# Optimization experiments

Hardware: AMD Instinct MI355X
Metric: run time of the kernel (lower is better)

## Reference

```python
import jax, jax.numpy as jnp
import numpy as np
import math

B, S, DIN = 8, 2048, 64
D, G, OUT_SEQ = 64, 5, 512
LN_EPS = 1e-5


def setup_inputs() -> dict:
    key = jax.random.key(0)
    ks = jax.random.split(key, 4)
    seq = jax.random.normal(ks[0], (B, S, DIN), dtype=jnp.float32)
    M = jax.random.uniform(ks[1], (D, DIN), minval=-0.5, maxval=0.5, dtype=jnp.float32)
    P = jax.random.uniform(ks[2], (D, D, G), minval=-0.1, maxval=0.1, dtype=jnp.float32)
    Linker = jax.random.uniform(ks[3], (S, OUT_SEQ), minval=-0.1, maxval=0.1, dtype=jnp.float32)
    ln_gamma = jnp.ones((D,), dtype=jnp.float32)
    ln_beta = jnp.zeros((D,), dtype=jnp.float32)
    return {"seq": seq, "M": M, "P": P, "Linker": Linker, "ln_gamma": ln_gamma, "ln_beta": ln_beta}


def _layer_norm(x, gamma, beta):
    mu = jnp.mean(x, axis=-1, keepdims=True)
    var = jnp.mean(jnp.square(x - mu), axis=-1, keepdims=True)
    return (x - mu) * jax.lax.rsqrt(var + LN_EPS) * gamma + beta


def reference(seq, M, P, Linker, ln_gamma, ln_beta):
    # periods[i,j,g] = i*(D*G) + j*G + g + 2 (constant buffer)
    periods = (jnp.arange(D * D * G, dtype=jnp.float32) + 2.0).reshape(D, D, G)
    k = jnp.arange(S, dtype=jnp.float32)
    # phi: (S, D, D, G) cosine basis
    phi = jnp.cos(2.0 * math.pi * k[:, None, None, None] / periods)
    # Precontract basis: W[k,i,j] = sum_g P[i,j,g] * phi[k,i,j,g]  -> (S, D, D)
    W = jnp.einsum('kijg,ijg->kij', phi, P)

    Z0 = jnp.einsum('bsd,od->bso', seq, M)          # x @ M^T, (B,S,D)
    Z = _layer_norm(Z0, ln_gamma, ln_beta)          # (B,S,D)
    # T[b,k,i] = sum_j Z[b,k,j] * W[k,i,j]
    T = jnp.einsum('bkj,kij->bki', Z, W)            # (B,S,D)
    U = jnp.einsum('bki,ko->boi', T, Linker)        # (B,OUT_SEQ,D)
    # shared residual: (x @ M^T)^T @ Linker, using pre-LayerNorm projection
    residual = jnp.einsum('bki,ko->boi', Z0, Linker)
    return U + residual
```

## Files before the change

kernel.cpp:

```cpp
#include <hip/hip_runtime.h>
#include <math.h>

#define SS 2048
#define OSQ 512
#define GG 5

typedef unsigned short u16;
typedef unsigned int u32;
typedef __attribute__((ext_vector_type(8))) short s16x8;
typedef __attribute__((ext_vector_type(4))) float v4f;
typedef __attribute__((ext_vector_type(16))) float v16f;

__device__ __forceinline__ float rcp_f(float x) {
    float r; asm("v_rcp_f32 %0, %1" : "=v"(r) : "v"(x)); return r;
}
__device__ __forceinline__ float cos_rev(float x) {
    float fr, c;
    asm("v_fract_f32 %0, %1" : "=v"(fr) : "v"(x));
    asm("v_cos_f32 %0, %1" : "=v"(c) : "v"(fr));
    return c;
}
__device__ __forceinline__ float cos01(float x) {
    float c; asm("v_cos_f32 %0, %1" : "=v"(c) : "v"(x)); return c;
}
__device__ __forceinline__ u16 f2bf(float f) {
    u32 u = __float_as_uint(f);
    return (u16)((u + 0x7FFFu + ((u >> 16) & 1u)) >> 16);
}
__device__ __forceinline__ float bf2f(u16 h) {
    return __uint_as_float((u32)h << 16);
}
__device__ __forceinline__ void gload16(const void* g, void* l) {
    __builtin_amdgcn_global_load_lds((const __attribute__((address_space(1))) void*)g,
                                     (__attribute__((address_space(3))) void*)l, 16, 0, 0);
}


__global__ __launch_bounds__(512, 1) void kF(const float* __restrict__ seq,
                                             const float* __restrict__ Mm,
                                             const float* __restrict__ P,
                                             const float* __restrict__ gamma,
                                             const float* __restrict__ beta,
                                             const float* __restrict__ Lnk,
                                             u16* __restrict__ Lt,
                                             u16* __restrict__ Vt) {
    __shared__ __align__(16) u16 SEQb[64 * 64];
    __shared__ __align__(16) u16 Mb[64 * 64];
    __shared__ __align__(16) u16 SZb[64 * 64];
    __shared__ float Z0l[64 * 68];
    __shared__ u32 Ta32[8 * 2 * 64 * 5];

    const int t = threadIdx.x;
    const int l = t & 63;
    const int w = t >> 6;
    const int k0 = blockIdx.x * 8;
    const float kf0 = (float)k0;

    const int h = w >> 2;
    const int i0 = (w & 3) * 16;
    const int i_w = i0 + (l & 15);
    const int jc_w = h * 4 + (l >> 4);

    float pr[40];
    {
        const float4* P4 = (const float4*)(P + ((size_t)i_w * 64 + jc_w * 8) * 5);
        #pragma unroll
        for (int q = 0; q < 10; ++q) {
            float4 v = P4[q];
            pr[q * 4 + 0] = v.x; pr[q * 4 + 1] = v.y; pr[q * 4 + 2] = v.z; pr[q * 4 + 3] = v.w;
        }
    }

    float lnv[8];
    #pragma unroll
    for (int j = 0; j < 8; ++j)
        lnv[j] = Lnk[(size_t)(k0 + j) * OSQ + t];

    {
        int row = t >> 3, ch = t & 7;
        int b = row >> 3, kq = row & 7;
        const float* sp = &seq[((size_t)b * SS + k0 + kq) * 64 + ch * 8];
        float4 a = *(const float4*)sp, bb4 = *(const float4*)(sp + 4);
        uint4 pk;
        pk.x = (u32)f2bf(a.x) | ((u32)f2bf(a.y) << 16);
        pk.y = (u32)f2bf(a.z) | ((u32)f2bf(a.w) << 16);
        pk.z = (u32)f2bf(bb4.x) | ((u32)f2bf(bb4.y) << 16);
        pk.w = (u32)f2bf(bb4.z) | ((u32)f2bf(bb4.w) << 16);
        *(uint4*)&SEQb[row * 64 + ((ch ^ (row & 7)) * 8)] = pk;

        const float* mp = &Mm[(size_t)row * 64 + ch * 8];
        float4 c = *(const float4*)mp, d = *(const float4*)(mp + 4);
        uint4 pm;
        pm.x = (u32)f2bf(c.x) | ((u32)f2bf(c.y) << 16);
        pm.y = (u32)f2bf(c.z) | ((u32)f2bf(c.w) << 16);
        pm.z = (u32)f2bf(d.x) | ((u32)f2bf(d.y) << 16);
        pm.w = (u32)f2bf(d.z) | ((u32)f2bf(d.w) << 16);
        *(uint4*)&Mb[row * 64 + ((ch ^ (row & 7)) * 8)] = pm;
    }

    float c0[40], c1[40], t2c[40];
    #pragma unroll
    for (int m = 0; m < 8; ++m) {
        #pragma unroll
        for (int g = 0; g < GG; ++g) {
            int idx = m * 5 + g;
            float pf = (float)((i_w * 64 + jc_w * 8 + m) * 5 + g + 2);
            float inv = rcp_f(pf);
            c0[idx] = cos_rev(kf0 * inv);
            c1[idx] = cos_rev((kf0 + 1.0f) * inv);
            float ct = cos01(inv);
            t2c[idx] = ct + ct;
        }
    }

    float gm[8], bt[8];
    {
        int oc = t & 7;
        float4 a = *(const float4*)&gamma[oc * 8], b = *(const float4*)&gamma[oc * 8 + 4];
        float4 c = *(const float4*)&beta[oc * 8],  d = *(const float4*)&beta[oc * 8 + 4];
        gm[0]=a.x; gm[1]=a.y; gm[2]=a.z; gm[3]=a.w; gm[4]=b.x; gm[5]=b.y; gm[6]=b.z; gm[7]=b.w;
        bt[0]=c.x; bt[1]=c.y; bt[2]=c.z; bt[3]=c.w; bt[4]=d.x; bt[5]=d.y; bt[6]=d.z; bt[7]=d.w;
    }
    __syncthreads();

    if (w < 4) {
        const int qr = w & 1, qc = w >> 1;
        v16f acc = {0,0,0,0,0,0,0,0,0,0,0,0,0,0,0,0};
        const int rowA = qr * 32 + (l & 31);
        const int rowB = qc * 32 + (l & 31);
        #pragma unroll
        for (int ks = 0; ks < 4; ++ks) {
            int cA = (ks * 2 + (l >> 5)) ^ (rowA & 7);
            int cB = (ks * 2 + (l >> 5)) ^ (rowB & 7);
            s16x8 af = *(const s16x8*)&SEQb[rowA * 64 + cA * 8];
            s16x8 bf = *(const s16x8*)&Mb[rowB * 64 + cB * 8];
            acc = __builtin_amdgcn_mfma_f32_32x32x16_bf16(af, bf, acc, 0, 0, 0);
        }
        #pragma unroll
        for (int q = 0; q < 16; ++q) {
            int row = qr * 32 + (q & 3) + 8 * (q >> 2) + 4 * (l >> 5);
            int col = qc * 32 + (l & 31);
            Z0l[row * 68 + col] = acc[q];
        }
    }
    __syncthreads();

    {
        const int rI = t >> 3, oc = t & 7;
        float z0v[8];
        float4 a = *(const float4*)&Z0l[rI * 68 + oc * 8];
        float4 b = *(const float4*)&Z0l[rI * 68 + oc * 8 + 4];
        z0v[0]=a.x; z0v[1]=a.y; z0v[2]=a.z; z0v[3]=a.w; z0v[4]=b.x; z0v[5]=b.y; z0v[6]=b.z; z0v[7]=b.w;
        float s1 = ((z0v[0]+z0v[1])+(z0v[2]+z0v[3])) + ((z0v[4]+z0v[5])+(z0v[6]+z0v[7]));
        s1 += __shfl_xor(s1, 1); s1 += __shfl_xor(s1, 2); s1 += __shfl_xor(s1, 4);
        float mu = s1 * 0.015625f;
        float sq = 0.f;
        #pragma unroll
        for (int m = 0; m < 8; ++m) { float dv = z0v[m] - mu; sq = fmaf(dv, dv, sq); }
        sq += __shfl_xor(sq, 1); sq += __shfl_xor(sq, 2); sq += __shfl_xor(sq, 4);
        float rstd = rsqrtf(sq * 0.015625f + 1e-5f);
        u16 zb[8];
        #pragma unroll
        for (int m = 0; m < 8; ++m)
            zb[m] = f2bf(fmaf((z0v[m] - mu) * rstd, gm[m], bt[m]));
        uint4 pk;
        pk.x = (u32)zb[0] | ((u32)zb[1] << 16);
        pk.y = (u32)zb[2] | ((u32)zb[3] << 16);
        pk.z = (u32)zb[4] | ((u32)zb[5] << 16);
        pk.w = (u32)zb[6] | ((u32)zb[7] << 16);
        int slot = oc ^ ((rI >> 3) & 7);
        *(uint4*)&SZb[rI * 64 + slot * 8] = pk;
    }
    __syncthreads();

    const int bcl = l & 7;
    #pragma unroll
    for (int kc = 0; kc < 8; ++kc) {
        if (kc >= 2) {
            #pragma unroll
            for (int x = 0; x < 40; ++x) {
                float cn = fmaf(t2c[x], c1[x], -c0[x]);
                c0[x] = c1[x]; c1[x] = cn;
            }
        }
        s16x8 bw;
        #pragma unroll
        for (int j = 0; j < 8; ++j) {
            float a = 0.f;
            #pragma unroll
            for (int g = 0; g < GG; ++g) {
                float ph = (kc == 0) ? c0[j * 5 + g] : c1[j * 5 + g];
                a = fmaf(pr[j * 5 + g], ph, a);
            }
            bw[j] = (short)f2bf(a);
        }
        int arow = bcl * 8 + kc;
        int slot = (h * 4 + (l >> 4)) ^ bcl;
        s16x8 az = *(const s16x8*)&SZb[arow * 64 + slot * 8];
        v4f zc = {0.f, 0.f, 0.f, 0.f};
        v4f d = __builtin_amdgcn_mfma_f32_16x16x32_bf16(az, bw, zc, 0, 0, 0);
        if (l < 32) {
            int ii = i0 + (l & 15);
            int bb2 = (l >> 4) * 2;
            u32 base = (u32)((kc * 2 + h) * 64 + ii) * 5 + bb2;
            Ta32[base]     = (u32)f2bf(d[0]) | ((u32)f2bf(d[1]) << 16);
            Ta32[base + 1] = (u32)f2bf(d[2]) | ((u32)f2bf(d[3]) << 16);
        }
    }
    __syncthreads();

    {
        const u16* TaR = (const u16*)Ta32;
        float vk[8];
        #pragma unroll
        for (int kc = 0; kc < 8; ++kc)
            vk[kc] = bf2f(TaR[((kc * 2 + 0) * 64 + l) * 10 + w])
                   + bf2f(TaR[((kc * 2 + 1) * 64 + l) * 10 + w])
                   + Z0l[(w * 8 + kc) * 68 + l];
        uint4 pk;
        pk.x = (u32)f2bf(vk[0]) | ((u32)f2bf(vk[1]) << 16);
        pk.y = (u32)f2bf(vk[2]) | ((u32)f2bf(vk[3]) << 16);
        pk.z = (u32)f2bf(vk[4]) | ((u32)f2bf(vk[5]) << 16);
        pk.w = (u32)f2bf(vk[6]) | ((u32)f2bf(vk[7]) << 16);
        const int ks = k0 >> 4;
        const int hi = (k0 >> 3) & 1;
        size_t idx16 = ((size_t)(w * 2 + (l >> 5)) * 128 + ks) * 64 + (l & 31) + 32 * hi;
        *(uint4*)&Vt[idx16 * 8] = pk;
    }

    {
        uint4 pk;
        pk.x = (u32)f2bf(lnv[0]) | ((u32)f2bf(lnv[1]) << 16);
        pk.y = (u32)f2bf(lnv[2]) | ((u32)f2bf(lnv[3]) << 16);
        pk.z = (u32)f2bf(lnv[4]) | ((u32)f2bf(lnv[5]) << 16);
        pk.w = (u32)f2bf(lnv[6]) | ((u32)f2bf(lnv[7]) << 16);
        const int ks = k0 >> 4;
        const int hi = (k0 >> 3) & 1;
        size_t idx16 = ((size_t)(t >> 5) * 128 + ks) * 64 + (t & 31) + 32 * hi;
        *(uint4*)&Lt[idx16 * 8] = pk;
    }
}

__global__ __launch_bounds__(256, 2) void kB2(const u16* __restrict__ Lt,
                                              const u16* __restrict__ Vt,
                                              float* __restrict__ out) {
    __shared__ __align__(16) u16 LB[4][2][2][2048];
    const int t = threadIdx.x;
    const int l = t & 63, w = t >> 6;
    const int p = blockIdx.x;
    const int lg = (p & 7) * 32 + (p >> 3);
    const int it = lg & 1, ot = (lg >> 1) & 15, b = lg >> 5;

    const u16* aG = Lt + (((size_t)ot * 128 + w * 32) * 64 + l) * 8;
    const u16* bG = Vt + (((size_t)(b * 2 + it) * 128 + w * 32) * 64 + l) * 8;

    v16f acc0 = {0,0,0,0,0,0,0,0,0,0,0,0,0,0,0,0};
    v16f acc1 = acc0;

#define STAGE(c, buf)                                                          \
    {                                                                          \
        _Pragma("unroll")                                                      \
        for (int ksl = 0; ksl < 4; ++ksl) {                                    \
            gload16(aG + ((c) * 4 + ksl) * 512, &LB[w][buf][0][ksl * 512]);    \
            gload16(bG + ((c) * 4 + ksl) * 512, &LB[w][buf][1][ksl * 512]);    \
        }                                                                      \
    }

    STAGE(0, 0);
    STAGE(1, 1);
    #pragma unroll
    for (int c = 0; c < 8; ++c) {
        if (c < 7) { asm volatile("s_waitcnt vmcnt(8)" ::: "memory"); }
        else       { asm volatile("s_waitcnt vmcnt(0)" ::: "memory"); }
        __builtin_amdgcn_sched_barrier(0);
        const int buf = c & 1;
        #pragma unroll
        for (int ksl = 0; ksl < 4; ++ksl) {
            s16x8 A = *(const s16x8*)&LB[w][buf][0][ksl * 512 + l * 8];
            s16x8 B = *(const s16x8*)&LB[w][buf][1][ksl * 512 + l * 8];
            if (ksl & 1) acc1 = __builtin_amdgcn_mfma_f32_32x32x16_bf16(A, B, acc1, 0, 0, 0);
            else         acc0 = __builtin_amdgcn_mfma_f32_32x32x16_bf16(A, B, acc0, 0, 0, 0);
        }
        asm volatile("s_waitcnt lgkmcnt(0)" ::: "memory");
        __builtin_amdgcn_sched_barrier(0);
        if (c + 2 < 8) STAGE(c + 2, buf);
    }
#undef STAGE

    __syncthreads();
    float* red = (float*)LB;
    {
        const int base = (w * 64 + l) * 17;
        #pragma unroll
        for (int r = 0; r < 16; ++r) red[base + r] = acc0[r] + acc1[r];
    }
    __syncthreads();
    {
        const int icol = t & 31;
        const int ob = (t >> 5) * 4;
        #pragma unroll
        for (int q = 0; q < 4; ++q) {
            const int orow = ob + q;
            const int hi = (orow >> 2) & 1;
            const int r = (orow & 3) | ((orow >> 3) << 2);
            const int lp = icol + 32 * hi;
            float s = red[(0 * 64 + lp) * 17 + r] + red[(1 * 64 + lp) * 17 + r]
                    + red[(2 * 64 + lp) * 17 + r] + red[(3 * 64 + lp) * 17 + r];
            out[((size_t)b * OSQ + ot * 32 + orow) * 64 + it * 32 + icol] = s;
        }
    }
}

extern "C" void kernel_launch(void* const* d_in, const int* in_sizes, int n_in,
                              void* d_out, int out_size, void* d_ws, size_t ws_size,
                              hipStream_t stream) {
    const float* seq   = (const float*)d_in[0];
    const float* Mm    = (const float*)d_in[1];
    const float* P     = (const float*)d_in[2];
    const float* Lnk   = (const float*)d_in[3];
    const float* gamma = (const float*)d_in[4];
    const float* beta  = (const float*)d_in[5];

    u16* Lt = (u16*)d_ws;
    u16* Vt = (u16*)((char*)d_ws + (2u << 20));

    kF<<<256, 512, 0, stream>>>(seq, Mm, P, gamma, beta, Lnk, Lt, Vt);
    kB2<<<256, 256, 0, stream>>>(Lt, Vt, (float*)d_out);
}
```

Before: 21.67 us.

## Halve per-block k-range in kF and double grid to 512 blocks

The first kernel now processes 4 sequence positions per block instead of 8, launching 512 blocks with launch bounds raised to allow 2 blocks per CU. Basis weights are generated in two halves of 4 j-values each, and the results are staged in packed registers before the MFMA loop, to lower register pressure. The aim is more parallelism and occupancy to cover the cosine/recurrence latency. In exchange, each block recomputes the P loads and cosine setup for half as much work, and the output stores become narrower 8-byte writes.

```diff
diff --git a/kernel.cpp b/kernel.cpp
--- a/kernel.cpp
+++ b/kernel.cpp
@@ -27,6 +27,9 @@
     u32 u = __float_as_uint(f);
     return (u16)((u + 0x7FFFu + ((u >> 16) & 1u)) >> 16);
 }
+__device__ __forceinline__ u32 pk2bf(float lo, float hi) {
+    return (u32)f2bf(lo) | ((u32)f2bf(hi) << 16);
+}
 __device__ __forceinline__ float bf2f(u16 h) {
     return __uint_as_float((u32)h << 16);
 }
@@ -36,7 +39,7 @@
 }
 
 
-__global__ __launch_bounds__(512, 1) void kF(const float* __restrict__ seq,
+__global__ __launch_bounds__(512, 2) void kF(const float* __restrict__ seq,
                                              const float* __restrict__ Mm,
                                              const float* __restrict__ P,
                                              const float* __restrict__ gamma,
@@ -44,16 +47,16 @@
                                              const float* __restrict__ Lnk,
                                              u16* __restrict__ Lt,
                                              u16* __restrict__ Vt) {
-    __shared__ __align__(16) u16 SEQb[64 * 64];
+    __shared__ __align__(16) u16 SEQb[32 * 64];
     __shared__ __align__(16) u16 Mb[64 * 64];
-    __shared__ __align__(16) u16 SZb[64 * 64];
-    __shared__ float Z0l[64 * 68];
-    __shared__ u32 Ta32[8 * 2 * 64 * 5];
+    __shared__ __align__(16) u16 SZb[32 * 64];
+    __shared__ float Z0l[32 * 68];
+    __shared__ u32 Ta32[4 * 2 * 64 * 5];
 
     const int t = threadIdx.x;
     const int l = t & 63;
     const int w = t >> 6;
-    const int k0 = blockIdx.x * 8;
+    const int k0 = blockIdx.x * 4;
     const float kf0 = (float)k0;
 
     const int h = w >> 2;
@@ -61,56 +64,33 @@
     const int i_w = i0 + (l & 15);
     const int jc_w = h * 4 + (l >> 4);
 
-    float pr[40];
-    {
-        const float4* P4 = (const float4*)(P + ((size_t)i_w * 64 + jc_w * 8) * 5);
-        #pragma unroll
-        for (int q = 0; q < 10; ++q) {
-            float4 v = P4[q];
-            pr[q * 4 + 0] = v.x; pr[q * 4 + 1] = v.y; pr[q * 4 + 2] = v.z; pr[q * 4 + 3] = v.w;
-        }
-    }
-
-    float lnv[8];
+    float lnv[4];
     #pragma unroll
-    for (int j = 0; j < 8; ++j)
+    for (int j = 0; j < 4; ++j)
         lnv[j] = Lnk[(size_t)(k0 + j) * OSQ + t];
 
-    {
+    if (t < 256) {
         int row = t >> 3, ch = t & 7;
-        int b = row >> 3, kq = row & 7;
+        int b = row >> 2, kq = row & 3;
         const float* sp = &seq[((size_t)b * SS + k0 + kq) * 64 + ch * 8];
         float4 a = *(const float4*)sp, bb4 = *(const float4*)(sp + 4);
         uint4 pk;
-        pk.x = (u32)f2bf(a.x) | ((u32)f2bf(a.y) << 16);
-        pk.y = (u32)f2bf(a.z) | ((u32)f2bf(a.w) << 16);
-        pk.z = (u32)f2bf(bb4.x) | ((u32)f2bf(bb4.y) << 16);
-        pk.w = (u32)f2bf(bb4.z) | ((u32)f2bf(bb4.w) << 16);
+        pk.x = pk2bf(a.x, a.y);
+        pk.y = pk2bf(a.z, a.w);
+        pk.z = pk2bf(bb4.x, bb4.y);
+        pk.w = pk2bf(bb4.z, bb4.w);
         *(uint4*)&SEQb[row * 64 + ((ch ^ (row & 7)) * 8)] = pk;
-
+    }
+    {
+        int row = t >> 3, ch = t & 7;
         const float* mp = &Mm[(size_t)row * 64 + ch * 8];
         float4 c = *(const float4*)mp, d = *(const float4*)(mp + 4);
         uint4 pm;
-        pm.x = (u32)f2bf(c.x) | ((u32)f2bf(c.y) << 16);
-        pm.y = (u32)f2bf(c.z) | ((u32)f2bf(c.w) << 16);
-        pm.z = (u32)f2bf(d.x) | ((u32)f2bf(d.y) << 16);
-        pm.w = (u32)f2bf(d.z) | ((u32)f2bf(d.w) << 16);
+        pm.x = pk2bf(c.x, c.y);
+        pm.y = pk2bf(c.z, c.w);
+        pm.z = pk2bf(d.x, d.y);
+        pm.w = pk2bf(d.z, d.w);
         *(uint4*)&Mb[row * 64 + ((ch ^ (row & 7)) * 8)] = pm;
-    }
-
-    float c0[40], c1[40], t2c[40];
-    #pragma unroll
-    for (int m = 0; m < 8; ++m) {
-        #pragma unroll
-        for (int g = 0; g < GG; ++g) {
-            int idx = m * 5 + g;
-            float pf = (float)((i_w * 64 + jc_w * 8 + m) * 5 + g + 2);
-            float inv = rcp_f(pf);
-            c0[idx] = cos_rev(kf0 * inv);
-            c1[idx] = cos_rev((kf0 + 1.0f) * inv);
-            float ct = cos01(inv);
-            t2c[idx] = ct + ct;
-        }
     }
 
     float gm[8], bt[8];
@@ -123,11 +103,10 @@
     }
     __syncthreads();
 
-    if (w < 4) {
-        const int qr = w & 1, qc = w >> 1;
+    if (w < 2) {
         v16f acc = {0,0,0,0,0,0,0,0,0,0,0,0,0,0,0,0};
-        const int rowA = qr * 32 + (l & 31);
-        const int rowB = qc * 32 + (l & 31);
+        const int rowA = l & 31;
+        const int rowB = w * 32 + (l & 31);
         #pragma unroll
         for (int ks = 0; ks < 4; ++ks) {
             int cA = (ks * 2 + (l >> 5)) ^ (rowA & 7);
@@ -138,14 +117,14 @@
         }
         #pragma unroll
         for (int q = 0; q < 16; ++q) {
-            int row = qr * 32 + (q & 3) + 8 * (q >> 2) + 4 * (l >> 5);
-            int col = qc * 32 + (l & 31);
+            int row = (q & 3) + 8 * (q >> 2) + 4 * (l >> 5);
+            int col = w * 32 + (l & 31);
             Z0l[row * 68 + col] = acc[q];
         }
     }
     __syncthreads();
 
-    {
+    if (t < 256) {
         const int rI = t >> 3, oc = t & 7;
         float z0v[8];
         float4 a = *(const float4*)&Z0l[rI * 68 + oc * 8];
@@ -159,85 +138,113 @@
         for (int m = 0; m < 8; ++m) { float dv = z0v[m] - mu; sq = fmaf(dv, dv, sq); }
         sq += __shfl_xor(sq, 1); sq += __shfl_xor(sq, 2); sq += __shfl_xor(sq, 4);
         float rstd = rsqrtf(sq * 0.015625f + 1e-5f);
-        u16 zb[8];
-        #pragma unroll
-        for (int m = 0; m < 8; ++m)
-            zb[m] = f2bf(fmaf((z0v[m] - mu) * rstd, gm[m], bt[m]));
         uint4 pk;
-        pk.x = (u32)zb[0] | ((u32)zb[1] << 16);
-        pk.y = (u32)zb[2] | ((u32)zb[3] << 16);
-        pk.z = (u32)zb[4] | ((u32)zb[5] << 16);
-        pk.w = (u32)zb[6] | ((u32)zb[7] << 16);
-        int slot = oc ^ ((rI >> 3) & 7);
+        pk.x = pk2bf(fmaf((z0v[0]-mu)*rstd, gm[0], bt[0]), fmaf((z0v[1]-mu)*rstd, gm[1], bt[1]));
+        pk.y = pk2bf(fmaf((z0v[2]-mu)*rstd, gm[2], bt[2]), fmaf((z0v[3]-mu)*rstd, gm[3], bt[3]));
+        pk.z = pk2bf(fmaf((z0v[4]-mu)*rstd, gm[4], bt[4]), fmaf((z0v[5]-mu)*rstd, gm[5], bt[5]));
+        pk.w = pk2bf(fmaf((z0v[6]-mu)*rstd, gm[6], bt[6]), fmaf((z0v[7]-mu)*rstd, gm[7], bt[7]));
+        int slot = oc ^ ((rI >> 2) & 7);
         *(uint4*)&SZb[rI * 64 + slot * 8] = pk;
     }
     __syncthreads();
+
+    u32 bwst[4][4];
+    #pragma unroll
+    for (int jh = 0; jh < 2; ++jh) {
+        float prh[20];
+        {
+            const float4* P4 = (const float4*)(P + ((size_t)i_w * 64 + jc_w * 8 + jh * 4) * 5);
+            #pragma unroll
+            for (int q = 0; q < 5; ++q) {
+                float4 v = P4[q];
+                prh[q*4+0] = v.x; prh[q*4+1] = v.y; prh[q*4+2] = v.z; prh[q*4+3] = v.w;
+            }
+        }
+        float c0[20], c1[20], t2c[20];
+        #pragma unroll
+        for (int m = 0; m < 4; ++m) {
+            #pragma unroll
+            for (int g = 0; g < GG; ++g) {
+                int idx = m * 5 + g;
+                float pf = (float)((i_w * 64 + jc_w * 8 + jh * 4 + m) * 5 + g + 2);
+                float inv = rcp_f(pf);
+                c0[idx] = cos_rev(kf0 * inv);
+                c1[idx] = cos_rev((kf0 + 1.0f) * inv);
+                float ct = cos01(inv);
+                t2c[idx] = ct + ct;
+            }
+        }
+        #pragma unroll
+        for (int kc = 0; kc < 4; ++kc) {
+            if (kc >= 2) {
+                #pragma unroll
+                for (int x = 0; x < 20; ++x) {
+                    float cn = fmaf(t2c[x], c1[x], -c0[x]);
+                    c0[x] = c1[x]; c1[x] = cn;
+                }
+            }
+            float av[4];
+            #pragma unroll
+            for (int m = 0; m < 4; ++m) {
+                float a = 0.f;
+                #pragma unroll
+                for (int g = 0; g < GG; ++g) {
+                    float ph = (kc == 0) ? c0[m * 5 + g] : c1[m * 5 + g];
+                    a = fmaf(prh[m * 5 + g], ph, a);
+                }
+                av[m] = a;
+            }
+            bwst[kc][jh * 2 + 0] = pk2bf(av[0], av[1]);
+            bwst[kc][jh * 2 + 1] = pk2bf(av[2], av[3]);
+        }
+    }
 
     const int bcl = l & 7;
     #pragma unroll
-    for (int kc = 0; kc < 8; ++kc) {
-        if (kc >= 2) {
-            #pragma unroll
-            for (int x = 0; x < 40; ++x) {
-                float cn = fmaf(t2c[x], c1[x], -c0[x]);
-                c0[x] = c1[x]; c1[x] = cn;
-            }
-        }
-        s16x8 bw;
-        #pragma unroll
-        for (int j = 0; j < 8; ++j) {
-            float a = 0.f;
-            #pragma unroll
-            for (int g = 0; g < GG; ++g) {
-                float ph = (kc == 0) ? c0[j * 5 + g] : c1[j * 5 + g];
-                a = fmaf(pr[j * 5 + g], ph, a);
-            }
-            bw[j] = (short)f2bf(a);
-        }
-        int arow = bcl * 8 + kc;
+    for (int kc = 0; kc < 4; ++kc) {
+        union { uint4 u; s16x8 v; } bwu;
+        bwu.u.x = bwst[kc][0]; bwu.u.y = bwst[kc][1];
+        bwu.u.z = bwst[kc][2]; bwu.u.w = bwst[kc][3];
+        int arow = bcl * 4 + kc;
         int slot = (h * 4 + (l >> 4)) ^ bcl;
         s16x8 az = *(const s16x8*)&SZb[arow * 64 + slot * 8];
         v4f zc = {0.f, 0.f, 0.f, 0.f};
-        v4f d = __builtin_amdgcn_mfma_f32_16x16x32_bf16(az, bw, zc, 0, 0, 0);
+        v4f d = __builtin_amdgcn_mfma_f32_16x16x32_bf16(az, bwu.v, zc, 0, 0, 0);
         if (l < 32) {
             int ii = i0 + (l & 15);
             int bb2 = (l >> 4) * 2;
             u32 base = (u32)((kc * 2 + h) * 64 + ii) * 5 + bb2;
-            Ta32[base]     = (u32)f2bf(d[0]) | ((u32)f2bf(d[1]) << 16);
-            Ta32[base + 1] = (u32)f2bf(d[2]) | ((u32)f2bf(d[3]) << 16);
-        }
-    }
-    __syncthreads();
+            Ta32[base]     = pk2bf(d[0], d[1]);
+            Ta32[base + 1] = pk2bf(d[2], d[3]);
+        }
+    }
+    __syncthreads();
+
+    const int ks = k0 >> 4;
+    const int hi = (k0 >> 3) & 1;
+    const int ofs = k0 & 4;
 
     {
         const u16* TaR = (const u16*)Ta32;
-        float vk[8];
-        #pragma unroll
-        for (int kc = 0; kc < 8; ++kc)
+        float vk[4];
+        #pragma unroll
+        for (int kc = 0; kc < 4; ++kc)
             vk[kc] = bf2f(TaR[((kc * 2 + 0) * 64 + l) * 10 + w])
                    + bf2f(TaR[((kc * 2 + 1) * 64 + l) * 10 + w])
-                   + Z0l[(w * 8 + kc) * 68 + l];
-        uint4 pk;
-        pk.x = (u32)f2bf(vk[0]) | ((u32)f2bf(vk[1]) << 16);
-        pk.y = (u32)f2bf(vk[2]) | ((u32)f2bf(vk[3]) << 16);
-        pk.z = (u32)f2bf(vk[4]) | ((u32)f2bf(vk[5]) << 16);
-        pk.w = (u32)f2bf(vk[6]) | ((u32)f2bf(vk[7]) << 16);
-        const int ks = k0 >> 4;
-        const int hi = (k0 >> 3) & 1;
+                   + Z0l[(w * 4 + kc) * 68 + l];
+        uint2 pk2;
+        pk2.x = pk2bf(vk[0], vk[1]);
+        pk2.y = pk2bf(vk[2], vk[3]);
         size_t idx16 = ((size_t)(w * 2 + (l >> 5)) * 128 + ks) * 64 + (l & 31) + 32 * hi;
-        *(uint4*)&Vt[idx16 * 8] = pk;
-    }
-
-    {
-        uint4 pk;
-        pk.x = (u32)f2bf(lnv[0]) | ((u32)f2bf(lnv[1]) << 16);
-        pk.y = (u32)f2bf(lnv[2]) | ((u32)f2bf(lnv[3]) << 16);
-        pk.z = (u32)f2bf(lnv[4]) | ((u32)f2bf(lnv[5]) << 16);
-        pk.w = (u32)f2bf(lnv[6]) | ((u32)f2bf(lnv[7]) << 16);
-        const int ks = k0 >> 4;
-        const int hi = (k0 >> 3) & 1;
+        *(uint2*)&Vt[idx16 * 8 + ofs] = pk2;
+    }
+
+    {
+        uint2 pk2;
+        pk2.x = pk2bf(lnv[0], lnv[1]);
+        pk2.y = pk2bf(lnv[2], lnv[3]);
         size_t idx16 = ((size_t)(t >> 5) * 128 + ks) * 64 + (t & 31) + 32 * hi;
-        *(uint4*)&Lt[idx16 * 8] = pk;
+        *(uint2*)&Lt[idx16 * 8 + ofs] = pk2;
     }
 }
 
@@ -324,6 +331,6 @@
     u16* Lt = (u16*)d_ws;
     u16* Vt = (u16*)((char*)d_ws + (2u << 20));
 
-    kF<<<256, 512, 0, stream>>>(seq, Mm, P, gamma, beta, Lnk, Lt, Vt);
+    kF<<<512, 512, 0, stream>>>(seq, Mm, P, gamma, beta, Lnk, Lt, Vt);
     kB2<<<256, 256, 0, stream>>>(Lt, Vt, (float*)d_out);
 }
```

Result: slower. 28.60 us (+32.0%).
